# Kernel optimization log

Measured on AMD Instinct MI355X. Metric: run time of the kernel, lower is better.

Reference implementation:

```python
import jax, jax.numpy as jnp
import numpy as np

B, S, D_IN = 1, 2048, 2048
H, KV, HD = 32, 8, 64          # num_heads, num_kv_groups, head_dim
GS = H // KV                    # group_size
D_OUT = H * HD
EPS = 1e-6


def _rmsnorm(x, w):
    # RMSNormQwen over last dim (head_dim)
    var = jnp.mean(x * x, axis=-1, keepdims=True)
    return x * jax.lax.rsqrt(var + EPS) * w


def _rope(x, cos, sin):
    # rotate-half RoPE; x: [B, heads, S, HD], cos/sin: [S, HD]
    d = x.shape[-1]
    x1, x2 = x[..., : d // 2], x[..., d // 2 :]
    rot = jnp.concatenate([-x2, x1], axis=-1)
    return x * cos + rot * sin


def setup_inputs() -> dict:
    key = jax.random.key(0)
    ks = jax.random.split(key, 8)
    x = jax.random.normal(ks[0], (B, S, D_IN), dtype=jnp.float32)
    Wq = jax.random.normal(ks[1], (D_IN, D_OUT), dtype=jnp.float32) * 0.02
    Wk = jax.random.normal(ks[2], (D_IN, KV * HD), dtype=jnp.float32) * 0.02
    Wv = jax.random.normal(ks[3], (D_IN, KV * HD), dtype=jnp.float32) * 0.02
    Wo = jax.random.normal(ks[4], (D_OUT, D_IN), dtype=jnp.float32) * 0.02
    q_norm_w = jnp.ones((HD,), dtype=jnp.float32)
    k_norm_w = jnp.ones((HD,), dtype=jnp.float32)
    # causal mask: True where masked (j > i)
    mask = jnp.triu(jnp.ones((S, S), dtype=bool), k=1)
    # RoPE tables
    inv_freq = 1.0 / (10000.0 ** (np.arange(0, HD, 2, dtype=np.float32) / HD))
    ang = np.arange(S, dtype=np.float32)[:, None] * inv_freq[None, :]  # [S, HD/2]
    cos = jnp.asarray(np.concatenate([np.cos(ang), np.cos(ang)], axis=-1))
    sin = jnp.asarray(np.concatenate([np.sin(ang), np.sin(ang)], axis=-1))
    return {"x": x, "mask": mask, "cos": cos, "sin": sin,
            "Wq": Wq, "Wk": Wk, "Wv": Wv, "Wo": Wo,
            "q_norm_w": q_norm_w, "k_norm_w": k_norm_w}


def reference(x, mask, cos, sin, Wq, Wk, Wv, Wo, q_norm_w, k_norm_w):
    b, s, _ = x.shape
    q = (x @ Wq).reshape(b, s, H, HD).transpose(0, 2, 1, 3)   # [B,H,S,HD]
    k = (x @ Wk).reshape(b, s, KV, HD).transpose(0, 2, 1, 3)  # [B,KV,S,HD]
    v = (x @ Wv).reshape(b, s, KV, HD).transpose(0, 2, 1, 3)  # [B,KV,S,HD]
    q = _rmsnorm(q, q_norm_w)
    k = _rmsnorm(k, k_norm_w)
    q = _rope(q, cos, sin)
    k = _rope(k, cos, sin)
    # grouped-KV attention without materializing repeated K/V
    qg = q.reshape(b, KV, GS, s, HD)
    scores = jnp.einsum('bkgsd,bktd->bkgst', qg, k)           # [B,KV,GS,S,S]
    scores = jnp.where(mask, -jnp.inf, scores)
    weights = jax.nn.softmax(scores / (HD ** 0.5), axis=-1)
    ctx = jnp.einsum('bkgst,bktd->bkgsd', weights, v)         # [B,KV,GS,S,HD]
    ctx = ctx.reshape(b, H, s, HD).transpose(0, 2, 1, 3).reshape(b, s, D_OUT)
    return ctx @ Wo
```

## Files before the change

### kernel.cpp

```cpp
#include <hip/hip_runtime.h>
#include <hip/hip_bf16.h>
#include <math.h>

#define S_LEN 2048
#define DIN   2048
#define NH    32
#define NKV   8
#define HD    64
#define DOUT  2048
#define QKVN  3072
#define KOFF  2048
#define VOFF  2560

typedef __attribute__((ext_vector_type(8))) short short8v;
typedef __attribute__((ext_vector_type(8))) unsigned short ushort8v;
typedef __attribute__((ext_vector_type(4))) unsigned short ushort4v;
typedef __attribute__((ext_vector_type(4))) float float4v;
typedef __attribute__((ext_vector_type(16))) float float16v;

__device__ __forceinline__ float bf2f(unsigned short u) {
    union { float f; unsigned u; } c; c.u = ((unsigned)u) << 16; return c.f;
}
__device__ __forceinline__ unsigned short f2bf(float f) {
    union { float f; unsigned u; } c; c.f = f;
    unsigned r = c.u + 0x7fffu + ((c.u >> 16) & 1u);
    return (unsigned short)(r >> 16);
}
__device__ __forceinline__ unsigned short f2h(float f) {
    union { _Float16 h; unsigned short u; } c; c.h = (_Float16)f; return c.u;
}
__device__ __forceinline__ float h2f(unsigned short u) {
    union { _Float16 h; unsigned short u; } c; c.u = u; return (float)c.h;
}
__device__ __forceinline__ unsigned cvtpk(float lo, float hi) {
    unsigned r;
    asm("v_cvt_pk_bf16_f32 %0, %1, %2" : "=v"(r) : "v"(lo), "v"(hi));
    return r;
}

__global__ __launch_bounds__(256) void prep(const float* __restrict__ Wq,
                                            const float* __restrict__ Wk,
                                            const float* __restrict__ Wv,
                                            const float* __restrict__ Wo,
                                            const float* __restrict__ x,
                                            unsigned short* __restrict__ W1,
                                            unsigned short* __restrict__ WoT,
                                            unsigned short* __restrict__ XB) {
    __shared__ float t[32][33];
    const int a = blockIdx.x;
    const int tx = threadIdx.x & 31, ty = threadIdx.x >> 5;
    if (a < 6144) {
        const int n0 = (a % 96) * 32, k0 = (a / 96) * 32;
        const float* src; int nn0, Nsrc;
        if (n0 < KOFF)      { src = Wq; nn0 = n0;        Nsrc = DOUT; }
        else if (n0 < VOFF) { src = Wk; nn0 = n0 - KOFF; Nsrc = 512; }
        else                { src = Wv; nn0 = n0 - VOFF; Nsrc = 512; }
#pragma unroll
        for (int j = ty; j < 32; j += 8)
            t[j][tx] = src[(size_t)(k0 + j) * Nsrc + nn0 + tx];
        __syncthreads();
#pragma unroll
        for (int j = ty; j < 32; j += 8)
            W1[(size_t)(n0 + j) * DIN + k0 + tx] = f2bf(t[tx][j]);
    } else if (a < 10240) {
        const int b = a - 6144;
        const int n0 = (b % 64) * 32, k0 = (b / 64) * 32;
#pragma unroll
        for (int j = ty; j < 32; j += 8)
            t[j][tx] = Wo[(size_t)(k0 + j) * DIN + n0 + tx];
        __syncthreads();
#pragma unroll
        for (int j = ty; j < 32; j += 8)
            WoT[(size_t)(n0 + j) * DOUT + k0 + tx] = f2bf(t[tx][j]);
    } else {
        const int i = (a - 10240) * 1024 + threadIdx.x * 4;
        float4 v = *(const float4*)(x + i);
        XB[i + 0] = f2bf(v.x); XB[i + 1] = f2bf(v.y);
        XB[i + 2] = f2bf(v.z); XB[i + 3] = f2bf(v.w);
    }
}

template <int FUSE>
__global__ __launch_bounds__(256) void gemm64(const unsigned short* __restrict__ A,
                                              const unsigned short* __restrict__ Bt,
                                              void* __restrict__ Cv, int M, int N, int K,
                                              const float* __restrict__ qnw,
                                              const float* __restrict__ knw,
                                              const float* __restrict__ cosb,
                                              const float* __restrict__ sinb) {
    __shared__ __attribute__((aligned(16))) unsigned short As[2 * 128 * 64];
    __shared__ __attribute__((aligned(16))) unsigned short Bs[2 * 64 * 64];
    const int tid = threadIdx.x, lane = tid & 63, w = tid >> 6;
    const int bm = blockIdx.y * 128, bn = blockIdx.x * 64;
    const int wm = w * 32;

    float4v acc[2][4];
#pragma unroll
    for (int i = 0; i < 2; i++)
#pragma unroll
        for (int j = 0; j < 4; j++) acc[i][j] = (float4v){0.f, 0.f, 0.f, 0.f};

    const int srow = lane >> 3;
    const int schk = (lane & 7) ^ srow;
    const unsigned short* Ag[4];
    const unsigned short* Bg[2];
#pragma unroll
    for (int g = 0; g < 4; g++)
        Ag[g] = A + (size_t)(bm + w * 32 + g * 8 + srow) * K + schk * 8;
#pragma unroll
    for (int g = 0; g < 2; g++)
        Bg[g] = Bt + (size_t)(bn + w * 16 + g * 8 + srow) * K + schk * 8;

    auto STAGE = [&](int t, int b) {
        const size_t ko = (size_t)t * 64;
        unsigned short* Ad = As + b * (128 * 64) + (w * 32) * 64;
        unsigned short* Bd = Bs + b * (64 * 64) + (w * 16) * 64;
#pragma unroll
        for (int g = 0; g < 4; g++)
            __builtin_amdgcn_global_load_lds(
                (const __attribute__((address_space(1))) void*)(Ag[g] + ko),
                (__attribute__((address_space(3))) void*)(Ad + g * 8 * 64), 16, 0, 0);
#pragma unroll
        for (int g = 0; g < 2; g++)
            __builtin_amdgcn_global_load_lds(
                (const __attribute__((address_space(1))) void*)(Bg[g] + ko),
                (__attribute__((address_space(3))) void*)(Bd + g * 8 * 64), 16, 0, 0);
    };

    const int frow = lane & 15, quad = lane >> 4, sw = frow & 7;
    const int NT = K >> 6;

    STAGE(0, 0);

    for (int t = 0; t < NT; t++) {
        const int c = t & 1;
        if (t + 1 < NT) {
            STAGE(t + 1, c ^ 1);
            asm volatile("s_waitcnt vmcnt(6)" ::: "memory");
        } else {
            asm volatile("s_waitcnt vmcnt(0)" ::: "memory");
        }
        __builtin_amdgcn_s_barrier();
        __builtin_amdgcn_sched_barrier(0);

        const unsigned short* Ab = As + c * (128 * 64);
        const unsigned short* Bb = Bs + c * (64 * 64);
        short8v af[2][2], bf[4][2];
#pragma unroll
        for (int fm = 0; fm < 2; fm++)
#pragma unroll
            for (int ks = 0; ks < 2; ks++)
                af[fm][ks] = *(const short8v*)(Ab + (wm + fm * 16 + frow) * 64 +
                                               (((ks * 4 + quad) ^ sw) * 8));
#pragma unroll
        for (int fn = 0; fn < 4; fn++)
#pragma unroll
            for (int ks = 0; ks < 2; ks++)
                bf[fn][ks] = *(const short8v*)(Bb + (fn * 16 + frow) * 64 +
                                               (((ks * 4 + quad) ^ sw) * 8));
        __builtin_amdgcn_s_setprio(1);
#pragma unroll
        for (int ks = 0; ks < 2; ks++)
#pragma unroll
            for (int fm = 0; fm < 2; fm++)
#pragma unroll
                for (int fn = 0; fn < 4; fn++)
                    acc[fm][fn] = __builtin_amdgcn_mfma_f32_16x16x32_bf16(
                        af[fm][ks], bf[fn][ks], acc[fm][fn], 0, 0, 0);
        __builtin_amdgcn_s_setprio(0);

        if (t + 1 < NT) {
            asm volatile("s_waitcnt lgkmcnt(0)" ::: "memory");
            __builtin_amdgcn_sched_barrier(0);
            __builtin_amdgcn_s_barrier();
        }
    }

    const int quad4 = lane >> 4, col16 = lane & 15;
    if constexpr (FUSE == 1) {
        unsigned short* C = (unsigned short*)Cv;
        const int head = bn >> 6;
        if (head < 40) {
            const float* nw = (head < 32) ? qnw : knw;
            float wv[4];
#pragma unroll
            for (int fn = 0; fn < 4; fn++) wv[fn] = nw[fn * 16 + col16];
#pragma unroll
            for (int fm = 0; fm < 2; fm++)
#pragma unroll
                for (int r = 0; r < 4; r++) {
                    float x0 = acc[fm][0][r], x1 = acc[fm][1][r];
                    float x2 = acc[fm][2][r], x3 = acc[fm][3][r];
                    float ss = x0 * x0 + x1 * x1 + x2 * x2 + x3 * x3;
                    ss += __shfl_xor(ss, 1); ss += __shfl_xor(ss, 2);
                    ss += __shfl_xor(ss, 4); ss += __shfl_xor(ss, 8);
                    const float inv = rsqrtf(ss * (1.0f / 64.0f) + 1e-6f);
                    float xn[4] = {x0 * inv * wv[0], x1 * inv * wv[1],
                                   x2 * inv * wv[2], x3 * inv * wv[3]};
                    const int row = bm + wm + fm * 16 + quad4 * 4 + r;
                    const float* cr = cosb + (size_t)row * HD;
                    const float* sr = sinb + (size_t)row * HD;
#pragma unroll
                    for (int fn = 0; fn < 4; fn++) {
                        const float rot = (fn < 2) ? -xn[fn + 2] : xn[fn - 2];
                        const float res = xn[fn] * cr[fn * 16 + col16] +
                                          rot * sr[fn * 16 + col16];
                        C[(size_t)row * N + bn + fn * 16 + col16] = f2bf(res);
                    }
                }
        } else {
#pragma unroll
            for (int fm = 0; fm < 2; fm++)
#pragma unroll
                for (int fn = 0; fn < 4; fn++)
#pragma unroll
                    for (int r = 0; r < 4; r++)
                        C[(size_t)(bm + wm + fm * 16 + quad4 * 4 + r) * N +
                          bn + fn * 16 + col16] = f2bf(acc[fm][fn][r]);
        }
    } else {
        float* C = (float*)Cv;
#pragma unroll
        for (int fm = 0; fm < 2; fm++)
#pragma unroll
            for (int fn = 0; fn < 4; fn++)
#pragma unroll
                for (int r = 0; r < 4; r++)
                    C[(size_t)(bm + wm + fm * 16 + quad4 * 4 + r) * N +
                      bn + fn * 16 + col16] = acc[fm][fn][r];
    }
}

#define KSTR 88

__global__ __launch_bounds__(256) void flash_part(const unsigned short* __restrict__ qb,
                                                  const unsigned short* __restrict__ kb,
                                                  const unsigned short* __restrict__ vb,
                                                  unsigned short* __restrict__ Op,
                                                  float* __restrict__ Lp) {
    __shared__ __attribute__((aligned(16))) unsigned short Ks[2][64 * KSTR];
    __shared__ __attribute__((aligned(16))) unsigned short Vt[2][64 * KSTR];

    const int tid = threadIdx.x, lane = tid & 63, w = tid >> 6;
    const int sl = lane & 31, hi = lane >> 5, hi8 = hi * 8;
    const int bid = blockIdx.x;
    const int g = bid & 7;
    const int p = (bid >> 3) & 31;
    const int s = bid >> 8;
    const int h = g * 4 + w;

    const int s0a = p * 32, s0b = (63 - p) * 32;
    const int nta = (s0a + 95) >> 6;
    const int nA  = s ? 0 : nta;
    const int bLo = s ? (17 - nta) : 0;
    const int nB  = s ? 16 : (17 - nta);
    const int nT  = nA + nB;

    const float C1 = 0.18033688011112042f;
    const float C2 = 12.262908856239697f;

    unsigned short* Oh = Op + (size_t)s * S_LEN * DOUT;
    float* Lh = Lp + (size_t)s * S_LEN * NH;

    int s0 = nA ? s0a : s0b;

    short8v qf[4], qfB[4];
#pragma unroll
    for (int ksq = 0; ksq < 4; ksq++)
        qf[ksq] = *(const short8v*)(qb + (size_t)(s0 + sl) * QKVN + h * HD +
                                    ksq * 16 + hi8);
    if (nA) {
#pragma unroll
        for (int ksq = 0; ksq < 4; ksq++)
            qfB[ksq] = *(const short8v*)(qb + (size_t)(s0b + sl) * QKVN + h * HD +
                                         ksq * 16 + hi8);
    }

    float16v O[2];
#pragma unroll
    for (int df = 0; df < 2; df++)
#pragma unroll
        for (int r = 0; r < 16; r++) O[df][r] = 0.f;
    float lsum = 0.f;

    const int kkey = tid >> 2, kch = tid & 3;
    const unsigned short* kg = kb + (size_t)kkey * QKVN + g * HD + kch * 16;
    const int kp = tid & 31, vdbb = tid >> 5;
    const unsigned short* vg0 = vb + (size_t)(2 * kp) * QKVN + g * HD + vdbb * 8;
    const unsigned short* vg1 = vg0 + QKVN;

    auto epi = [&](int sbase) {
        float lt = lsum + __shfl_xor(lsum, 32);
        if (hi == 0) Lh[(size_t)(sbase + sl) * NH + h] = lt;
#pragma unroll
        for (int df = 0; df < 2; df++)
#pragma unroll
            for (int r = 0; r < 16; r++) {
                const int row = sbase + (r & 3) + 8 * (r >> 2) + 4 * hi;
                Oh[(size_t)row * DOUT + h * HD + df * 32 + sl] = f2h(O[df][r]);
            }
    };

    auto tileIdx = [&](int j) { return (j < nA) ? j : (bLo + (j - nA)); };

    ushort8v ka0, ka1, va0, va1;
    auto LOADREGS = [&](int it) {
        const size_t off = (size_t)it * 64 * QKVN;
        ka0 = *(const ushort8v*)(kg + off);
        ka1 = *(const ushort8v*)(kg + off + 8);
        va0 = *(const ushort8v*)(vg0 + off);
        va1 = *(const ushort8v*)(vg1 + off);
    };
    auto COMMIT = [&](int b) {
        unsigned short* kd = Ks[b] + kkey * KSTR + kch * 16;
        *(ushort8v*)kd = ka0;
        *(ushort8v*)(kd + 8) = ka1;
        union { ushort8v v; unsigned d[4]; } ua, ub;
        ua.v = va0; ub.v = va1;
        unsigned short* vd = Vt[b] + (size_t)(vdbb * 8) * KSTR + 2 * kp;
#pragma unroll
        for (int i = 0; i < 8; i++) {
            const unsigned sel = (i & 1) ? 0x07060302u : 0x05040100u;
            const unsigned word = __builtin_amdgcn_perm(ub.d[i >> 1], ua.d[i >> 1], sel);
            *(unsigned*)(vd + (size_t)i * KSTR) = word;
        }
    };

    LOADREGS(tileIdx(0));
    COMMIT(0);
    if (nT > 1) LOADREGS(tileIdx(1));

    for (int j = 0; j < nT; j++) {
        const int cur = j & 1;
        __syncthreads();
        if (j + 1 < nT) COMMIT(cur ^ 1);
        if (j + 2 < nT) LOADREGS(tileIdx(j + 2));
        if (nA && j == nA) {
            epi(s0a);
#pragma unroll
            for (int df = 0; df < 2; df++)
#pragma unroll
                for (int r = 0; r < 16; r++) O[df][r] = 0.f;
            lsum = 0.f;
            s0 = s0b;
#pragma unroll
            for (int ksq = 0; ksq < 4; ksq++) qf[ksq] = qfB[ksq];
        }

        const int t0 = tileIdx(j) * 64;
        const bool edge = (t0 + 63 > s0);

#pragma unroll
        for (int b = 0; b < 2; b++) {
            short8v kf[4];
#pragma unroll
            for (int ksq = 0; ksq < 4; ksq++)
                kf[ksq] = *(const short8v*)(Ks[cur] + (32 * b + sl) * KSTR +
                                            ksq * 16 + hi8);
            float16v sct;
#pragma unroll
            for (int r = 0; r < 16; r++) sct[r] = 0.f;
            __builtin_amdgcn_s_setprio(1);
#pragma unroll
            for (int ksq = 0; ksq < 4; ksq++)
                sct = __builtin_amdgcn_mfma_f32_32x32x16_bf16(kf[ksq], qf[ksq],
                                                              sct, 0, 0, 0);
            __builtin_amdgcn_s_setprio(0);
#pragma unroll
            for (int r = 0; r < 16; r++) {
                float arg = sct[r] * C1 - C2;
                if (edge) {
                    const int kglob = t0 + 32 * b + (r & 3) + 8 * (r >> 2) + 4 * hi;
                    arg = (kglob <= s0 + sl) ? arg : -100.f;
                }
                const float pv = exp2f(arg);
                sct[r] = pv;
                lsum += pv;
            }
            unsigned pk[8];
#pragma unroll
            for (int i = 0; i < 8; i++) pk[i] = cvtpk(sct[2 * i], sct[2 * i + 1]);
#pragma unroll
            for (int kk = 0; kk < 2; kk++) {
                const unsigned x0 = pk[4 * kk + 0], x1 = pk[4 * kk + 1];
                const unsigned y0 = pk[4 * kk + 2], y1 = pk[4 * kk + 3];
                const unsigned a0 = __shfl_xor(x0, 32), a1 = __shfl_xor(x1, 32);
                const unsigned b0 = __shfl_xor(y0, 32), b1 = __shfl_xor(y1, 32);
                union { unsigned u[4]; short8v v; } pa;
                pa.u[0] = hi ? b0 : x0;
                pa.u[1] = hi ? b1 : x1;
                pa.u[2] = hi ? y0 : a0;
                pa.u[3] = hi ? y1 : a1;
                const int ks = 2 * b + kk;
                __builtin_amdgcn_s_setprio(1);
#pragma unroll
                for (int df = 0; df < 2; df++) {
                    const short8v vf = *(const short8v*)(Vt[cur] +
                                                         (size_t)(df * 32 + sl) * KSTR +
                                                         ks * 16 + hi8);
                    O[df] = __builtin_amdgcn_mfma_f32_32x32x16_bf16(pa.v, vf,
                                                                    O[df], 0, 0, 0);
                }
                __builtin_amdgcn_s_setprio(0);
            }
        }
    }

    epi(s0);
}

__global__ __launch_bounds__(256) void combine(unsigned short* O01,
                                               const float* __restrict__ Lp) {
    const int i4 = (blockIdx.x * 256 + threadIdx.x) * 4;
    const int srow = i4 >> 11, hh = (i4 & 2047) >> 6;
    float l = Lp[(size_t)srow * NH + hh];
    ushort4v o0 = *(const ushort4v*)(O01 + i4);
    float acc[4];
#pragma unroll
    for (int j = 0; j < 4; j++) acc[j] = h2f(o0[j]);
    if (srow >= 1024) {
        l += Lp[(size_t)S_LEN * NH + (size_t)srow * NH + hh];
        ushort4v o1 = *(const ushort4v*)(O01 + (size_t)S_LEN * DOUT + i4);
#pragma unroll
        for (int j = 0; j < 4; j++) acc[j] += h2f(o1[j]);
    }
    const float inv = 1.0f / l;
    ushort4v r;
#pragma unroll
    for (int j = 0; j < 4; j++) r[j] = f2bf(acc[j] * inv);
    *(ushort4v*)(O01 + i4) = r;
}

extern "C" void kernel_launch(void* const* d_in, const int* in_sizes, int n_in,
                              void* d_out, int out_size, void* d_ws, size_t ws_size,
                              hipStream_t stream) {
    const float* x    = (const float*)d_in[0];
    const float* cosb = (const float*)d_in[2];
    const float* sinb = (const float*)d_in[3];
    const float* Wq   = (const float*)d_in[4];
    const float* Wk   = (const float*)d_in[5];
    const float* Wv   = (const float*)d_in[6];
    const float* Wo   = (const float*)d_in[7];
    const float* qw   = (const float*)d_in[8];
    const float* kw   = (const float*)d_in[9];
    float* out = (float*)d_out;

    unsigned short* W1  = (unsigned short*)d_ws;
    unsigned short* XB  = W1 + (size_t)QKVN * DIN;
    unsigned short* WoT = XB + (size_t)S_LEN * DIN;
    unsigned short* QKV = WoT + (size_t)DIN * DOUT;
    unsigned short* Op  = (unsigned short*)d_ws;
    float*          Lp  = (float*)(Op + (size_t)2 * S_LEN * DOUT);
    unsigned short* CTX = Op;

    dim3 blk256(256);

    prep<<<dim3(14336), blk256, 0, stream>>>(Wq, Wk, Wv, Wo, x, W1, WoT, XB);

    gemm64<1><<<dim3(QKVN / 64, S_LEN / 128), blk256, 0, stream>>>(
        XB, W1, QKV, S_LEN, QKVN, DIN, qw, kw, cosb, sinb);

    flash_part<<<dim3(NKV * 32 * 2), blk256, 0, stream>>>(
        QKV, QKV + KOFF, QKV + VOFF, Op, Lp);

    combine<<<dim3(S_LEN * DOUT / 1024), blk256, 0, stream>>>(Op, Lp);

    gemm64<0><<<dim3(DIN / 64, S_LEN / 128), blk256, 0, stream>>>(
        CTX, WoT, out, S_LEN, DIN, DOUT, nullptr, nullptr, nullptr, nullptr);
}
```

Before: 236.6 us.

## Split flash attention into three equal KV chunks per block with MFMA row sums

Flash attention work is repartitioned from two uneven splits into three equal 11-tile KV chunks per (group, pair), launching 768 blocks so load is balanced and more CUs stay busy. Row sums are computed with an extra MFMA against a ones vector instead of scalar adds. The cross-half shuffles are replaced with v_permlane32_swap, and exp2 becomes raw v_exp_f32. The combine kernel now merges two or three partials and writes CTX into the QKV buffer, with partial sums staged in the output buffer. The costs are an extra MFMA per step, more partial-output traffic in combine, and a launch-bounds occupancy hint that may force register spilling.

```diff
diff --git a/kernel.cpp b/kernel.cpp
--- a/kernel.cpp
+++ b/kernel.cpp
@@ -35,6 +35,11 @@
 __device__ __forceinline__ unsigned cvtpk(float lo, float hi) {
     unsigned r;
     asm("v_cvt_pk_bf16_f32 %0, %1, %2" : "=v"(r) : "v"(lo), "v"(hi));
+    return r;
+}
+__device__ __forceinline__ float fexp2(float x) {
+    float r;
+    asm("v_exp_f32 %0, %1" : "=v"(r) : "v"(x));
     return r;
 }
 
@@ -233,11 +238,11 @@
 
 #define KSTR 88
 
-__global__ __launch_bounds__(256) void flash_part(const unsigned short* __restrict__ qb,
-                                                  const unsigned short* __restrict__ kb,
-                                                  const unsigned short* __restrict__ vb,
-                                                  unsigned short* __restrict__ Op,
-                                                  float* __restrict__ Lp) {
+__global__ __launch_bounds__(256, 3) void flash_part(const unsigned short* __restrict__ qb,
+                                                     const unsigned short* __restrict__ kb,
+                                                     const unsigned short* __restrict__ vb,
+                                                     unsigned short* __restrict__ Op,
+                                                     float* __restrict__ Lp) {
     __shared__ __attribute__((aligned(16))) unsigned short Ks[2][64 * KSTR];
     __shared__ __attribute__((aligned(16))) unsigned short Vt[2][64 * KSTR];
 
@@ -246,42 +251,44 @@
     const int bid = blockIdx.x;
     const int g = bid & 7;
     const int p = (bid >> 3) & 31;
-    const int s = bid >> 8;
+    const int c = bid >> 8;
     const int h = g * 4 + w;
 
     const int s0a = p * 32, s0b = (63 - p) * 32;
     const int nta = (s0a + 95) >> 6;
-    const int nA  = s ? 0 : nta;
-    const int bLo = s ? (17 - nta) : 0;
-    const int nB  = s ? 16 : (17 - nta);
-    const int nT  = nA + nB;
+    const int W0 = c * 11;
+    int nA = nta - W0;
+    nA = nA < 0 ? 0 : (nA > 11 ? 11 : nA);
+    const bool owesA = (c < 2);
 
     const float C1 = 0.18033688011112042f;
     const float C2 = 12.262908856239697f;
 
-    unsigned short* Oh = Op + (size_t)s * S_LEN * DOUT;
-    float* Lh = Lp + (size_t)s * S_LEN * NH;
-
-    int s0 = nA ? s0a : s0b;
-
-    short8v qf[4], qfB[4];
+    unsigned short* OhA = Op + (size_t)c * 1024 * DOUT;
+    float*          LhA = Lp + (size_t)c * 1024 * NH;
+    unsigned short* OhB = Op + (size_t)(2 + c) * 1024 * DOUT;
+    float*          LhB = Lp + (size_t)(2 + c) * 1024 * NH;
+
+    int seg = owesA ? 0 : 1;
+    int s0 = seg == 0 ? s0a : s0b;
+
+    short8v qf[4];
 #pragma unroll
     for (int ksq = 0; ksq < 4; ksq++)
         qf[ksq] = *(const short8v*)(qb + (size_t)(s0 + sl) * QKVN + h * HD +
                                     ksq * 16 + hi8);
-    if (nA) {
-#pragma unroll
-        for (int ksq = 0; ksq < 4; ksq++)
-            qfB[ksq] = *(const short8v*)(qb + (size_t)(s0b + sl) * QKVN + h * HD +
-                                         ksq * 16 + hi8);
-    }
-
-    float16v O[2];
+
+    float16v O[2], Lacc;
 #pragma unroll
     for (int df = 0; df < 2; df++)
 #pragma unroll
         for (int r = 0; r < 16; r++) O[df][r] = 0.f;
-    float lsum = 0.f;
+#pragma unroll
+    for (int r = 0; r < 16; r++) Lacc[r] = 0.f;
+
+    short8v ones;
+#pragma unroll
+    for (int i = 0; i < 8; i++) ones[i] = (short)0x3F80;
 
     const int kkey = tid >> 2, kch = tid & 3;
     const unsigned short* kg = kb + (size_t)kkey * QKVN + g * HD + kch * 16;
@@ -289,19 +296,35 @@
     const unsigned short* vg0 = vb + (size_t)(2 * kp) * QKVN + g * HD + vdbb * 8;
     const unsigned short* vg1 = vg0 + QKVN;
 
-    auto epi = [&](int sbase) {
-        float lt = lsum + __shfl_xor(lsum, 32);
-        if (hi == 0) Lh[(size_t)(sbase + sl) * NH + h] = lt;
+    auto epi = [&](int sbase, unsigned short* Os, float* Ls, int roff) {
 #pragma unroll
         for (int df = 0; df < 2; df++)
 #pragma unroll
             for (int r = 0; r < 16; r++) {
-                const int row = sbase + (r & 3) + 8 * (r >> 2) + 4 * hi;
-                Oh[(size_t)row * DOUT + h * HD + df * 32 + sl] = f2h(O[df][r]);
+                const int row = sbase + (r & 3) + 8 * (r >> 2) + 4 * hi - roff;
+                Os[(size_t)row * DOUT + h * HD + df * 32 + sl] = f2h(O[df][r]);
             }
+        if (sl == 0) {
+#pragma unroll
+            for (int r = 0; r < 16; r++) {
+                const int row = sbase + (r & 3) + 8 * (r >> 2) + 4 * hi - roff;
+                Ls[(size_t)row * NH + h] = Lacc[r];
+            }
+        }
     };
-
-    auto tileIdx = [&](int j) { return (j < nA) ? j : (bLo + (j - nA)); };
+    auto zacc = [&]() {
+#pragma unroll
+        for (int df = 0; df < 2; df++)
+#pragma unroll
+            for (int r = 0; r < 16; r++) O[df][r] = 0.f;
+#pragma unroll
+        for (int r = 0; r < 16; r++) Lacc[r] = 0.f;
+    };
+
+    auto kt = [&](int jj) {
+        const int sj = W0 + jj;
+        return (sj < nta) ? sj : (sj - nta);
+    };
 
     ushort8v ka0, ka1, va0, va1;
     auto LOADREGS = [&](int it) {
@@ -326,28 +349,27 @@
         }
     };
 
-    LOADREGS(tileIdx(0));
+    LOADREGS(kt(0));
     COMMIT(0);
-    if (nT > 1) LOADREGS(tileIdx(1));
-
-    for (int j = 0; j < nT; j++) {
-        const int cur = j & 1;
+    LOADREGS(kt(1));
+
+#pragma unroll 1
+    for (int jj = 0; jj < 11; jj++) {
+        const int cur = jj & 1;
         __syncthreads();
-        if (j + 1 < nT) COMMIT(cur ^ 1);
-        if (j + 2 < nT) LOADREGS(tileIdx(j + 2));
-        if (nA && j == nA) {
-            epi(s0a);
-#pragma unroll
-            for (int df = 0; df < 2; df++)
-#pragma unroll
-                for (int r = 0; r < 16; r++) O[df][r] = 0.f;
-            lsum = 0.f;
-            s0 = s0b;
-#pragma unroll
-            for (int ksq = 0; ksq < 4; ksq++) qf[ksq] = qfB[ksq];
-        }
-
-        const int t0 = tileIdx(j) * 64;
+        if (jj + 1 < 11) COMMIT(cur ^ 1);
+        if (jj + 2 < 11) LOADREGS(kt(jj + 2));
+        if (seg == 0 && jj == nA) {
+            epi(s0a, OhA, LhA, 0);
+            zacc();
+            s0 = s0b; seg = 1;
+#pragma unroll
+            for (int ksq = 0; ksq < 4; ksq++)
+                qf[ksq] = *(const short8v*)(qb + (size_t)(s0b + sl) * QKVN +
+                                            h * HD + ksq * 16 + hi8);
+        }
+
+        const int t0 = kt(jj) * 64;
         const bool edge = (t0 + 63 > s0);
 
 #pragma unroll
@@ -373,24 +395,19 @@
                     const int kglob = t0 + 32 * b + (r & 3) + 8 * (r >> 2) + 4 * hi;
                     arg = (kglob <= s0 + sl) ? arg : -100.f;
                 }
-                const float pv = exp2f(arg);
-                sct[r] = pv;
-                lsum += pv;
+                sct[r] = fexp2(arg);
             }
             unsigned pk[8];
 #pragma unroll
             for (int i = 0; i < 8; i++) pk[i] = cvtpk(sct[2 * i], sct[2 * i + 1]);
 #pragma unroll
             for (int kk = 0; kk < 2; kk++) {
-                const unsigned x0 = pk[4 * kk + 0], x1 = pk[4 * kk + 1];
-                const unsigned y0 = pk[4 * kk + 2], y1 = pk[4 * kk + 3];
-                const unsigned a0 = __shfl_xor(x0, 32), a1 = __shfl_xor(x1, 32);
-                const unsigned b0 = __shfl_xor(y0, 32), b1 = __shfl_xor(y1, 32);
+                unsigned x0 = pk[4 * kk + 0], x1 = pk[4 * kk + 1];
+                unsigned y0 = pk[4 * kk + 2], y1 = pk[4 * kk + 3];
+                asm("v_permlane32_swap_b32 %0, %1" : "+v"(x0), "+v"(y0));
+                asm("v_permlane32_swap_b32 %0, %1" : "+v"(x1), "+v"(y1));
                 union { unsigned u[4]; short8v v; } pa;
-                pa.u[0] = hi ? b0 : x0;
-                pa.u[1] = hi ? b1 : x1;
-                pa.u[2] = hi ? y0 : a0;
-                pa.u[3] = hi ? y1 : a1;
+                pa.u[0] = x0; pa.u[1] = x1; pa.u[2] = y0; pa.u[3] = y1;
                 const int ks = 2 * b + kk;
                 __builtin_amdgcn_s_setprio(1);
 #pragma unroll
@@ -401,34 +418,49 @@
                     O[df] = __builtin_amdgcn_mfma_f32_32x32x16_bf16(pa.v, vf,
                                                                     O[df], 0, 0, 0);
                 }
+                Lacc = __builtin_amdgcn_mfma_f32_32x32x16_bf16(pa.v, ones,
+                                                               Lacc, 0, 0, 0);
                 __builtin_amdgcn_s_setprio(0);
             }
         }
     }
 
-    epi(s0);
-}
-
-__global__ __launch_bounds__(256) void combine(unsigned short* O01,
-                                               const float* __restrict__ Lp) {
+    if (seg == 0) {
+        epi(s0a, OhA, LhA, 0);
+        zacc();
+    }
+    epi(s0b, OhB, LhB, 1024);
+}
+
+__global__ __launch_bounds__(256) void combine(const unsigned short* __restrict__ Op,
+                                               const float* __restrict__ Lp,
+                                               unsigned short* __restrict__ CTX) {
     const int i4 = (blockIdx.x * 256 + threadIdx.x) * 4;
-    const int srow = i4 >> 11, hh = (i4 & 2047) >> 6;
-    float l = Lp[(size_t)srow * NH + hh];
-    ushort4v o0 = *(const ushort4v*)(O01 + i4);
+    const int row = i4 >> 11, hh = (i4 & 2047) >> 6;
     float acc[4];
-#pragma unroll
-    for (int j = 0; j < 4; j++) acc[j] = h2f(o0[j]);
-    if (srow >= 1024) {
-        l += Lp[(size_t)S_LEN * NH + (size_t)srow * NH + hh];
-        ushort4v o1 = *(const ushort4v*)(O01 + (size_t)S_LEN * DOUT + i4);
-#pragma unroll
-        for (int j = 0; j < 4; j++) acc[j] += h2f(o1[j]);
+    float l;
+    if (row < 1024) {
+        ushort4v a0 = *(const ushort4v*)(Op + i4);
+        ushort4v a1 = *(const ushort4v*)(Op + (size_t)1024 * DOUT + i4);
+#pragma unroll
+        for (int j = 0; j < 4; j++) acc[j] = h2f(a0[j]) + h2f(a1[j]);
+        l = Lp[(size_t)row * NH + hh] + Lp[(size_t)(1024 + row) * NH + hh];
+    } else {
+        const size_t j4 = (size_t)(row - 1024) * DOUT + (i4 & 2047);
+        ushort4v b0 = *(const ushort4v*)(Op + (size_t)2 * 1024 * DOUT + j4);
+        ushort4v b1 = *(const ushort4v*)(Op + (size_t)3 * 1024 * DOUT + j4);
+        ushort4v b2 = *(const ushort4v*)(Op + (size_t)4 * 1024 * DOUT + j4);
+#pragma unroll
+        for (int j = 0; j < 4; j++) acc[j] = h2f(b0[j]) + h2f(b1[j]) + h2f(b2[j]);
+        const size_t lr = (size_t)(row - 1024) * NH + hh;
+        l = Lp[(size_t)2 * 1024 * NH + lr] + Lp[(size_t)3 * 1024 * NH + lr] +
+            Lp[(size_t)4 * 1024 * NH + lr];
     }
     const float inv = 1.0f / l;
     ushort4v r;
 #pragma unroll
     for (int j = 0; j < 4; j++) r[j] = f2bf(acc[j] * inv);
-    *(ushort4v*)(O01 + i4) = r;
+    *(ushort4v*)(CTX + i4) = r;
 }
 
 extern "C" void kernel_launch(void* const* d_in, const int* in_sizes, int n_in,
@@ -450,8 +482,8 @@
     unsigned short* WoT = XB + (size_t)S_LEN * DIN;
     unsigned short* QKV = WoT + (size_t)DIN * DOUT;
     unsigned short* Op  = (unsigned short*)d_ws;
-    float*          Lp  = (float*)(Op + (size_t)2 * S_LEN * DOUT);
-    unsigned short* CTX = Op;
+    float*          Lp  = (float*)d_out;
+    unsigned short* CTX = QKV;
 
     dim3 blk256(256);
 
@@ -460,10 +492,10 @@
     gemm64<1><<<dim3(QKVN / 64, S_LEN / 128), blk256, 0, stream>>>(
         XB, W1, QKV, S_LEN, QKVN, DIN, qw, kw, cosb, sinb);
 
-    flash_part<<<dim3(NKV * 32 * 2), blk256, 0, stream>>>(
+    flash_part<<<dim3(NKV * 32 * 3), blk256, 0, stream>>>(
         QKV, QKV + KOFF, QKV + VOFF, Op, Lp);
 
-    combine<<<dim3(S_LEN * DOUT / 1024), blk256, 0, stream>>>(Op, Lp);
+    combine<<<dim3(S_LEN * DOUT / 1024), blk256, 0, stream>>>(Op, Lp, CTX);
 
     gemm64<0><<<dim3(DIN / 64, S_LEN / 128), blk256, 0, stream>>>(
         CTX, WoT, out, S_LEN, DIN, DOUT, nullptr, nullptr, nullptr, nullptr);
```

New measurement: 235.4 us. No clear change (-0.5%).
